# Optimization experiments

Measured on AMD Instinct MI355X. Metric: run time of the kernel, lower is better.

## Reference

```python
import jax, jax.numpy as jnp
import numpy as np

NUM_CLASSES = 8
EPS = 1e-4  # variance epsilon from the original module
MARGIN = 1.0  # __init__ arg; unused in the forward math


def setup_inputs() -> dict:
    key = jax.random.key(0)
    kf, kl = jax.random.split(key)
    features = jax.random.normal(kf, (65536, 2, 256), dtype=jnp.float32)
    labels = jax.random.randint(kl, (65536,), 0, NUM_CLASSES)
    return {"features": features, "labels": labels}


def _loss(features, labels):
    B, V, D = features.shape
    # Views of each sample are stacked into the sample's class group
    X = features.reshape(B * V, D)              # [N, D]
    lab = jnp.repeat(labels, V)                 # [N]
    onehot = (lab[:, None] == jnp.arange(NUM_CLASSES)[None, :]).astype(X.dtype)  # [N, C]

    counts = onehot.sum(axis=0)                 # [C] per-class row counts (all > 1 by construction)
    sums = onehot.T @ X                         # [C, D]
    means = sums / counts[:, None]              # [C, D]
    e2 = onehot.T @ (X * X)                     # [C, D] per-class sum of squares
    # unbiased per-feature variance (torch.var default, ddof=1)
    var = (e2 - counts[:, None] * means * means) / (counts[:, None] - 1.0)
    std = jnp.sqrt(var + EPS)
    std_loss = jnp.sum(jnp.mean(jax.nn.relu(1.0 - std), axis=1))  # sum over classes of mean over features

    # Per-class covariance: cov_c = (X_c - mu_c)^T (X_c - mu_c) / (n_c - 1)
    #                             = (sum_c x x^T - n_c mu mu^T) / (n_c - 1)
    S = jnp.einsum('nc,nd,ne->cde', onehot, X, X)  # [C, D, D]
    cov = (S - counts[:, None, None] * means[:, :, None] * means[:, None, :]) / (
        counts[:, None, None] - 1.0)
    diag = jnp.diagonal(cov, axis1=1, axis2=2)      # [C, D]
    offdiag_sq = jnp.sum(cov * cov, axis=(1, 2)) - jnp.sum(diag * diag, axis=1)
    cov_loss = jnp.sum(offdiag_sq / D)

    return std_loss + cov_loss


def reference(features, labels):
    return _loss(features, labels)
```

## Files before the change

kernel.cpp:

```cpp
#include <hip/hip_runtime.h>
#include <stdint.h>


#define NCLS  8
#define D     256
#define CHUNK 1024
#define SEG   256
#define EPSF  1e-4f
#define TMAX  144

typedef __bf16 bf16x8 __attribute__((ext_vector_type(8)));
typedef float  f32x4  __attribute__((ext_vector_type(4)));

__device__ __forceinline__ unsigned short f2bf(float f) {
    unsigned int x = __float_as_uint(f);
    x += 0x7fffu + ((x >> 16) & 1u);
    return (unsigned short)(x >> 16);
}

__global__ void k_hist(const int* __restrict__ labels, int nlab, int vfac,
                       int* __restrict__ counts) {
    __shared__ int lc[NCLS];
    int t = threadIdx.x;
    if (t < NCLS) lc[t] = 0;
    __syncthreads();
    for (int i = blockIdx.x * blockDim.x + t; i < nlab; i += gridDim.x * blockDim.x)
        atomicAdd(&lc[labels[i] & 7], vfac);
    __syncthreads();
    if (t < NCLS && lc[t]) atomicAdd(&counts[t], lc[t]);
}

__global__ void k_offsets(const int* __restrict__ counts,
                          int* __restrict__ offsets, int* __restrict__ cursor) {
    if (threadIdx.x == 0) {
        int acc = 0;
        for (int c = 0; c < NCLS; ++c) { offsets[c] = acc; cursor[c] = acc; acc += counts[c]; }
    }
}

__global__ __launch_bounds__(256) void k_idx(
    const int* __restrict__ labels, int nrows, int vfac,
    int* __restrict__ cursor, int* __restrict__ idx)
{
    __shared__ int lcnt[NCLS], lbase[NCLS];
    int t = threadIdx.x;
    int row = blockIdx.x * SEG + t;
    if (t < NCLS) lcnt[t] = 0;
    __syncthreads();
    int c = 0, rk = 0;
    bool ok = (row < nrows);
    if (ok) {
        c = labels[row / vfac] & 7;
        rk = atomicAdd(&lcnt[c], 1);
    }
    __syncthreads();
    if (t < NCLS) lbase[t] = lcnt[t] ? atomicAdd(&cursor[t], lcnt[t]) : 0;
    __syncthreads();
    if (ok) idx[lbase[c] + rk] = row;
}

__global__ __launch_bounds__(512) void k_gram_g(
    const float* __restrict__ X, const int* __restrict__ idx,
    const int* __restrict__ counts, const int* __restrict__ offsets,
    float* __restrict__ part, float* __restrict__ csums)
{
    __shared__ __align__(16) unsigned char lds[64 * 256 * 2];

    int t = threadIdx.x;
    int lane = t & 63;
    int w = t >> 6;
    int wrow = w >> 1;
    int wcol = w & 1;
    int kblk = t & 15;
    int cblk = t >> 4;

    int nch[NCLS], ofch[NCLS];
    int T = 0;
    for (int c = 0; c < NCLS; ++c) {
        int n = counts[c];
        nch[c] = (n + CHUNK - 1) / CHUNK;
        ofch[c] = T;
        T += nch[c];
    }

    const f32x4 zf = {0.f, 0.f, 0.f, 0.f};

    for (int wk = blockIdx.x; wk < 2 * T; wk += gridDim.x) {
        int item = wk >> 1;
        int half = wk & 1;
        int c = 0;
        while (c < NCLS - 1 && item >= ofch[c + 1]) ++c;
        int chunk = item - ofch[c];
        int base = offsets[c] + chunk * CHUNK;
        int rows = min(CHUNK, counts[c] - chunk * CHUNK);
        int ntiles = (rows + 63) >> 6;

        f32x4 acc[4][4];
        #pragma unroll
        for (int i = 0; i < 4; ++i)
            #pragma unroll
            for (int j = 0; j < 4; ++j)
                #pragma unroll
                for (int r = 0; r < 4; ++r) acc[i][j][r] = 0.f;
        float sumv[8];
        #pragma unroll
        for (int q = 0; q < 8; ++q) sumv[q] = 0.f;

        uint4 R[4];
        f32x4 fa[4], fb[4];
        int idn[4];

        #pragma unroll
        for (int j = 0; j < 4; ++j) {
            int r = kblk * 4 + j;
            idn[j] = (r < rows) ? idx[base + r] : 0;
        }
        #pragma unroll
        for (int j = 0; j < 4; ++j) {
            int r = kblk * 4 + j;
            if (r < rows) {
                const float* rp = X + ((size_t)idn[j] << 8) + cblk * 8;
                fa[j] = *(const f32x4*)rp;
                fb[j] = *(const f32x4*)(rp + 4);
            } else { fa[j] = zf; fb[j] = zf; }
        }
        #pragma unroll
        for (int j = 0; j < 4; ++j) {
            int r = 64 + kblk * 4 + j;
            idn[j] = (r < rows) ? idx[base + r] : 0;
        }
        #pragma unroll
        for (int j = 0; j < 4; ++j) {
            #pragma unroll
            for (int q = 0; q < 4; ++q) { sumv[q] += fa[j][q]; sumv[4 + q] += fb[j][q]; }
            unsigned int w0 = (unsigned int)f2bf(fa[j][0]) | ((unsigned int)f2bf(fa[j][1]) << 16);
            unsigned int w1 = (unsigned int)f2bf(fa[j][2]) | ((unsigned int)f2bf(fa[j][3]) << 16);
            unsigned int w2 = (unsigned int)f2bf(fb[j][0]) | ((unsigned int)f2bf(fb[j][1]) << 16);
            unsigned int w3 = (unsigned int)f2bf(fb[j][2]) | ((unsigned int)f2bf(fb[j][3]) << 16);
            R[j] = make_uint4(w0, w1, w2, w3);
        }

        for (int kt = 0; kt < ntiles; ++kt) {
            __syncthreads();
            #pragma unroll
            for (int cc = 0; cc < 8; ++cc) {
                int wd = cc >> 1;
                int sh = (cc & 1) * 16;
                unsigned int e0 = (((const unsigned int*)&R[0])[wd] >> sh) & 0xffffu;
                unsigned int e1 = (((const unsigned int*)&R[1])[wd] >> sh) & 0xffffu;
                unsigned int e2 = (((const unsigned int*)&R[2])[wd] >> sh) & 0xffffu;
                unsigned int e3 = (((const unsigned int*)&R[3])[wd] >> sh) & 0xffffu;
                int ccol = cblk * 8 + cc;
                int byt = ccol * 128 + ((kblk * 8) ^ (cc << 4));
                *(uint2*)(lds + byt) = make_uint2(e0 | (e1 << 16), e2 | (e3 << 16));
            }
            __syncthreads();

            bool more = (kt + 1 < ntiles);
            if (more) {
                #pragma unroll
                for (int j = 0; j < 4; ++j) {
                    int r = (kt + 1) * 64 + kblk * 4 + j;
                    if (r < rows) {
                        const float* rp = X + ((size_t)idn[j] << 8) + cblk * 8;
                        fa[j] = *(const f32x4*)rp;
                        fb[j] = *(const f32x4*)(rp + 4);
                    } else { fa[j] = zf; fb[j] = zf; }
                }
            }
            int idf[4];
            #pragma unroll
            for (int j = 0; j < 4; ++j) {
                int r = (kt + 2) * 64 + kblk * 4 + j;
                idf[j] = (more && r < rows) ? idx[base + r] : 0;
            }
            __builtin_amdgcn_sched_barrier(0);

            #pragma unroll
            for (int ks = 0; ks < 2; ++ks) {
                int kb2 = ks * 64 + ((lane >> 4) << 4);
                int swz = (lane & 7) << 4;
                bf16x8 bfr[4];
                #pragma unroll
                for (int tj = 0; tj < 4; ++tj) {
                    int ccol = half * 128 + wcol * 64 + tj * 16 + (lane & 15);
                    bfr[tj] = __builtin_bit_cast(bf16x8,
                        *(const uint4*)(lds + ccol * 128 + (kb2 ^ swz)));
                }
                #pragma unroll
                for (int ti = 0; ti < 4; ++ti) {
                    int ccol = wrow * 64 + ti * 16 + (lane & 15);
                    bf16x8 af = __builtin_bit_cast(bf16x8,
                        *(const uint4*)(lds + ccol * 128 + (kb2 ^ swz)));
                    #pragma unroll
                    for (int tj = 0; tj < 4; ++tj)
                        acc[ti][tj] = __builtin_amdgcn_mfma_f32_16x16x32_bf16(
                            af, bfr[tj], acc[ti][tj], 0, 0, 0);
                }
            }

            if (more) {
                #pragma unroll
                for (int j = 0; j < 4; ++j) {
                    #pragma unroll
                    for (int q = 0; q < 4; ++q) { sumv[q] += fa[j][q]; sumv[4 + q] += fb[j][q]; }
                    unsigned int w0 = (unsigned int)f2bf(fa[j][0]) | ((unsigned int)f2bf(fa[j][1]) << 16);
                    unsigned int w1 = (unsigned int)f2bf(fa[j][2]) | ((unsigned int)f2bf(fa[j][3]) << 16);
                    unsigned int w2 = (unsigned int)f2bf(fb[j][0]) | ((unsigned int)f2bf(fb[j][1]) << 16);
                    unsigned int w3 = (unsigned int)f2bf(fb[j][2]) | ((unsigned int)f2bf(fb[j][3]) << 16);
                    R[j] = make_uint4(w0, w1, w2, w3);
                }
                #pragma unroll
                for (int j = 0; j < 4; ++j) idn[j] = idf[j];
            }
        }

        float* dst = part + (size_t)item * (D * D);
        #pragma unroll
        for (int ti = 0; ti < 4; ++ti) {
            int row0 = wrow * 64 + ti * 16 + ((lane >> 4) << 2);
            #pragma unroll
            for (int tj = 0; tj < 4; ++tj) {
                int col = half * 128 + wcol * 64 + tj * 16 + (lane & 15);
                #pragma unroll
                for (int r = 0; r < 4; ++r)
                    dst[(row0 + r) * D + col] = acc[ti][tj][r];
            }
        }

        #pragma unroll
        for (int s = 1; s < 16; s <<= 1)
            #pragma unroll
            for (int q = 0; q < 8; ++q)
                sumv[q] += __shfl_xor(sumv[q], s, 64);
        if (half == 0 && (t & 15) == 0) {
            float* cs = csums + (size_t)item * D + cblk * 8;
            #pragma unroll
            for (int q = 0; q < 8; ++q) cs[q] = sumv[q];
        }
        __syncthreads();
    }
}

__global__ __launch_bounds__(256) void k_gsum(
    const float* __restrict__ csums, const int* __restrict__ counts,
    float* __restrict__ gsums)
{
    int c = blockIdx.x;
    int i = threadIdx.x;
    int of = 0;
    for (int cc = 0; cc < c; ++cc) of += (counts[cc] + CHUNK - 1) / CHUNK;
    int nc = (counts[c] + CHUNK - 1) / CHUNK;
    float s = 0.f;
    for (int q = 0; q < nc; ++q) s += csums[(size_t)(of + q) * D + i];
    gsums[c * D + i] = s;
}

__global__ __launch_bounds__(256) void k_loss(
    const float* __restrict__ part, const float* __restrict__ gsums,
    const int* __restrict__ counts, float* __restrict__ out)
{
    __shared__ float red[256];
    int t = threadIdx.x;
    int nch[NCLS], ofch[NCLS];
    int T = 0;
    for (int c = 0; c < NCLS; ++c) {
        int n = counts[c];
        nch[c] = (n + CHUNK - 1) / CHUNK;
        ofch[c] = T;
        T += nch[c];
    }
    float local = 0.f;
    const int total = NCLS * D * D;
    for (int idx = blockIdx.x * blockDim.x + t; idx < total; idx += gridDim.x * blockDim.x) {
        int c = idx >> 16;
        int ij = idx & 0xffff;
        int i = ij >> 8, j = ij & 255;
        const float* p = part + (size_t)ofch[c] * (D * D) + ij;
        float s = 0.f;
        for (int q = 0; q < nch[c]; ++q) s += p[(size_t)q * (D * D)];
        float n  = (float)counts[c];
        float mi = gsums[c * D + i] / n;
        float mj = gsums[c * D + j] / n;
        float cov = (s - n * mi * mj) / (n - 1.f);
        float contrib;
        if (i == j) {
            float sd = sqrtf(cov + EPSF);
            contrib = fmaxf(1.f - sd, 0.f) * (1.f / (float)D);
        } else {
            contrib = cov * cov * (1.f / (float)D);
        }
        local += contrib;
    }
    red[t] = local;
    __syncthreads();
    for (int s = 128; s > 0; s >>= 1) {
        if (t < s) red[t] += red[t + s];
        __syncthreads();
    }
    if (t == 0) atomicAdd(out, red[0]);
}

extern "C" void kernel_launch(void* const* d_in, const int* in_sizes, int n_in,
                              void* d_out, int out_size, void* d_ws, size_t ws_size,
                              hipStream_t stream)
{
    const float* X      = (const float*)d_in[0];
    const int*   labels = (const int*)d_in[1];
    int nfeat = in_sizes[0];
    int nlab  = in_sizes[1];
    int nrows = nfeat / D;
    int vfac  = nrows / nlab;

    char* ws = (char*)d_ws;
    size_t off_idx   = 0;
    size_t sz_idx    = (size_t)nrows * 4;
    size_t off_part  = (off_idx + sz_idx + 255) & ~(size_t)255;
    size_t sz_part   = (size_t)TMAX * D * D * 4;
    size_t off_cs    = (off_part + sz_part + 255) & ~(size_t)255;
    size_t sz_cs     = (size_t)TMAX * D * 4;
    size_t off_gs    = (off_cs + sz_cs + 255) & ~(size_t)255;
    size_t sz_gs     = (size_t)NCLS * D * 4;
    size_t off_cnt   = (off_gs + sz_gs + 255) & ~(size_t)255;
    size_t off_ofs   = off_cnt + 64;
    size_t off_cur   = off_ofs + 64;

    int*   idx     = (int*)(ws + off_idx);
    float* part    = (float*)(ws + off_part);
    float* csums   = (float*)(ws + off_cs);
    float* gsums   = (float*)(ws + off_gs);
    int*   counts  = (int*)(ws + off_cnt);
    int*   offsets = (int*)(ws + off_ofs);
    int*   cursor  = (int*)(ws + off_cur);

    hipMemsetAsync(counts, 0, 64, stream);
    hipMemsetAsync(d_out, 0, (size_t)out_size * sizeof(float), stream);

    k_hist<<<64, 256, 0, stream>>>(labels, nlab, vfac, counts);
    k_offsets<<<1, 64, 0, stream>>>(counts, offsets, cursor);
    k_idx<<<(nrows + SEG - 1) / SEG, SEG, 0, stream>>>(labels, nrows, vfac, cursor, idx);
    k_gram_g<<<2 * TMAX, 512, 0, stream>>>(X, idx, counts, offsets, part, csums);
    k_gsum<<<NCLS, 256, 0, stream>>>(csums, counts, gsums);
    k_loss<<<512, 256, 0, stream>>>(part, gsums, counts, (float*)d_out);
}
```

Measured before the change: 125.8 us.

## Double-buffer LDS tiles in gram kernel to drop one barrier per k-step

The shared-memory staging buffer for the bf16 row tiles becomes double-buffered. Each iteration computes MFMAs from the current buffer while the next tile is converted and written into the other buffer, so only one __syncthreads per k-step is needed instead of two. Row-bounds branches on gathers are replaced by clamped indices plus masking after the load, which makes the loads unconditional. The cost is double the LDS footprint (64KB per block), which may reduce occupancy, plus extra redundant loads for tail rows.

```diff
diff --git a/kernel.cpp b/kernel.cpp
--- a/kernel.cpp
+++ b/kernel.cpp
@@ -64,7 +64,7 @@
     const int* __restrict__ counts, const int* __restrict__ offsets,
     float* __restrict__ part, float* __restrict__ csums)
 {
-    __shared__ __align__(16) unsigned char lds[64 * 256 * 2];
+    __shared__ __align__(16) unsigned char lds[2][64 * 256 * 2];
 
     int t = threadIdx.x;
     int lane = t & 63;
@@ -106,28 +106,23 @@
         #pragma unroll
         for (int q = 0; q < 8; ++q) sumv[q] = 0.f;
 
+        f32x4 fa[4], fb[4];
         uint4 R[4];
-        f32x4 fa[4], fb[4];
         int idn[4];
 
         #pragma unroll
         for (int j = 0; j < 4; ++j) {
             int r = kblk * 4 + j;
-            idn[j] = (r < rows) ? idx[base + r] : 0;
-        }
-        #pragma unroll
-        for (int j = 0; j < 4; ++j) {
-            int r = kblk * 4 + j;
-            if (r < rows) {
-                const float* rp = X + ((size_t)idn[j] << 8) + cblk * 8;
-                fa[j] = *(const f32x4*)rp;
-                fb[j] = *(const f32x4*)(rp + 4);
-            } else { fa[j] = zf; fb[j] = zf; }
+            int rid = idx[base + min(r, rows - 1)];
+            const float* rp = X + ((size_t)rid << 8) + cblk * 8;
+            fa[j] = *(const f32x4*)rp;
+            fb[j] = *(const f32x4*)(rp + 4);
+            if (r >= rows) { fa[j] = zf; fb[j] = zf; }
         }
         #pragma unroll
         for (int j = 0; j < 4; ++j) {
             int r = 64 + kblk * 4 + j;
-            idn[j] = (r < rows) ? idx[base + r] : 0;
+            idn[j] = idx[base + min(r, rows - 1)];
         }
         #pragma unroll
         for (int j = 0; j < 4; ++j) {
@@ -139,43 +134,98 @@
             unsigned int w3 = (unsigned int)f2bf(fb[j][2]) | ((unsigned int)f2bf(fb[j][3]) << 16);
             R[j] = make_uint4(w0, w1, w2, w3);
         }
-
-        for (int kt = 0; kt < ntiles; ++kt) {
-            __syncthreads();
-            #pragma unroll
-            for (int cc = 0; cc < 8; ++cc) {
-                int wd = cc >> 1;
-                int sh = (cc & 1) * 16;
-                unsigned int e0 = (((const unsigned int*)&R[0])[wd] >> sh) & 0xffffu;
-                unsigned int e1 = (((const unsigned int*)&R[1])[wd] >> sh) & 0xffffu;
-                unsigned int e2 = (((const unsigned int*)&R[2])[wd] >> sh) & 0xffffu;
-                unsigned int e3 = (((const unsigned int*)&R[3])[wd] >> sh) & 0xffffu;
-                int ccol = cblk * 8 + cc;
-                int byt = ccol * 128 + ((kblk * 8) ^ (cc << 4));
-                *(uint2*)(lds + byt) = make_uint2(e0 | (e1 << 16), e2 | (e3 << 16));
-            }
-            __syncthreads();
-
-            bool more = (kt + 1 < ntiles);
-            if (more) {
-                #pragma unroll
-                for (int j = 0; j < 4; ++j) {
-                    int r = (kt + 1) * 64 + kblk * 4 + j;
-                    if (r < rows) {
-                        const float* rp = X + ((size_t)idn[j] << 8) + cblk * 8;
-                        fa[j] = *(const f32x4*)rp;
-                        fb[j] = *(const f32x4*)(rp + 4);
-                    } else { fa[j] = zf; fb[j] = zf; }
-                }
-            }
-            int idf[4];
+        #pragma unroll
+        for (int cc = 0; cc < 8; ++cc) {
+            int wd = cc >> 1;
+            int sh = (cc & 1) * 16;
+            unsigned int e0 = (((const unsigned int*)&R[0])[wd] >> sh) & 0xffffu;
+            unsigned int e1 = (((const unsigned int*)&R[1])[wd] >> sh) & 0xffffu;
+            unsigned int e2 = (((const unsigned int*)&R[2])[wd] >> sh) & 0xffffu;
+            unsigned int e3 = (((const unsigned int*)&R[3])[wd] >> sh) & 0xffffu;
+            int ccol = cblk * 8 + cc;
+            int byt = ccol * 128 + ((kblk * 8) ^ (cc << 4));
+            *(uint2*)(&lds[0][0] + byt) = make_uint2(e0 | (e1 << 16), e2 | (e3 << 16));
+        }
+        __syncthreads();
+
+        int ntm1 = ntiles - 1;
+        for (int kt = 0; kt < ntm1; ++kt) {
+            int cur = kt & 1;
+            #pragma unroll
+            for (int j = 0; j < 4; ++j) {
+                const float* rp = X + ((size_t)idn[j] << 8) + cblk * 8;
+                fa[j] = *(const f32x4*)rp;
+                fb[j] = *(const f32x4*)(rp + 4);
+            }
+            int idnn[4];
             #pragma unroll
             for (int j = 0; j < 4; ++j) {
                 int r = (kt + 2) * 64 + kblk * 4 + j;
-                idf[j] = (more && r < rows) ? idx[base + r] : 0;
+                idnn[j] = idx[base + min(r, rows - 1)];
             }
             __builtin_amdgcn_sched_barrier(0);
 
+            {
+                const unsigned char* lb = &lds[0][0] + cur * 32768;
+                #pragma unroll
+                for (int ks = 0; ks < 2; ++ks) {
+                    int kb2 = ks * 64 + ((lane >> 4) << 4);
+                    int swz = (lane & 7) << 4;
+                    bf16x8 bfr[4];
+                    #pragma unroll
+                    for (int tj = 0; tj < 4; ++tj) {
+                        int ccol = half * 128 + wcol * 64 + tj * 16 + (lane & 15);
+                        bfr[tj] = __builtin_bit_cast(bf16x8,
+                            *(const uint4*)(lb + ccol * 128 + (kb2 ^ swz)));
+                    }
+                    #pragma unroll
+                    for (int ti = 0; ti < 4; ++ti) {
+                        int ccol = wrow * 64 + ti * 16 + (lane & 15);
+                        bf16x8 af = __builtin_bit_cast(bf16x8,
+                            *(const uint4*)(lb + ccol * 128 + (kb2 ^ swz)));
+                        #pragma unroll
+                        for (int tj = 0; tj < 4; ++tj)
+                            acc[ti][tj] = __builtin_amdgcn_mfma_f32_16x16x32_bf16(
+                                af, bfr[tj], acc[ti][tj], 0, 0, 0);
+                    }
+                }
+            }
+            __builtin_amdgcn_sched_barrier(0);
+
+            #pragma unroll
+            for (int j = 0; j < 4; ++j) {
+                int r = (kt + 1) * 64 + kblk * 4 + j;
+                if (r >= rows) { fa[j] = zf; fb[j] = zf; }
+                #pragma unroll
+                for (int q = 0; q < 4; ++q) { sumv[q] += fa[j][q]; sumv[4 + q] += fb[j][q]; }
+                unsigned int w0 = (unsigned int)f2bf(fa[j][0]) | ((unsigned int)f2bf(fa[j][1]) << 16);
+                unsigned int w1 = (unsigned int)f2bf(fa[j][2]) | ((unsigned int)f2bf(fa[j][3]) << 16);
+                unsigned int w2 = (unsigned int)f2bf(fb[j][0]) | ((unsigned int)f2bf(fb[j][1]) << 16);
+                unsigned int w3 = (unsigned int)f2bf(fb[j][2]) | ((unsigned int)f2bf(fb[j][3]) << 16);
+                R[j] = make_uint4(w0, w1, w2, w3);
+            }
+            {
+                unsigned char* wb = &lds[0][0] + (cur ^ 1) * 32768;
+                #pragma unroll
+                for (int cc = 0; cc < 8; ++cc) {
+                    int wd = cc >> 1;
+                    int sh = (cc & 1) * 16;
+                    unsigned int e0 = (((const unsigned int*)&R[0])[wd] >> sh) & 0xffffu;
+                    unsigned int e1 = (((const unsigned int*)&R[1])[wd] >> sh) & 0xffffu;
+                    unsigned int e2 = (((const unsigned int*)&R[2])[wd] >> sh) & 0xffffu;
+                    unsigned int e3 = (((const unsigned int*)&R[3])[wd] >> sh) & 0xffffu;
+                    int ccol = cblk * 8 + cc;
+                    int byt = ccol * 128 + ((kblk * 8) ^ (cc << 4));
+                    *(uint2*)(wb + byt) = make_uint2(e0 | (e1 << 16), e2 | (e3 << 16));
+                }
+            }
+            #pragma unroll
+            for (int j = 0; j < 4; ++j) idn[j] = idnn[j];
+            __syncthreads();
+        }
+
+        {
+            const unsigned char* lb = &lds[0][0] + (ntm1 & 1) * 32768;
             #pragma unroll
             for (int ks = 0; ks < 2; ++ks) {
                 int kb2 = ks * 64 + ((lane >> 4) << 4);
@@ -185,33 +235,18 @@
                 for (int tj = 0; tj < 4; ++tj) {
                     int ccol = half * 128 + wcol * 64 + tj * 16 + (lane & 15);
                     bfr[tj] = __builtin_bit_cast(bf16x8,
-                        *(const uint4*)(lds + ccol * 128 + (kb2 ^ swz)));
+                        *(const uint4*)(lb + ccol * 128 + (kb2 ^ swz)));
                 }
                 #pragma unroll
                 for (int ti = 0; ti < 4; ++ti) {
                     int ccol = wrow * 64 + ti * 16 + (lane & 15);
                     bf16x8 af = __builtin_bit_cast(bf16x8,
-                        *(const uint4*)(lds + ccol * 128 + (kb2 ^ swz)));
+                        *(const uint4*)(lb + ccol * 128 + (kb2 ^ swz)));
                     #pragma unroll
                     for (int tj = 0; tj < 4; ++tj)
                         acc[ti][tj] = __builtin_amdgcn_mfma_f32_16x16x32_bf16(
                             af, bfr[tj], acc[ti][tj], 0, 0, 0);
                 }
-            }
-
-            if (more) {
-                #pragma unroll
-                for (int j = 0; j < 4; ++j) {
-                    #pragma unroll
-                    for (int q = 0; q < 4; ++q) { sumv[q] += fa[j][q]; sumv[4 + q] += fb[j][q]; }
-                    unsigned int w0 = (unsigned int)f2bf(fa[j][0]) | ((unsigned int)f2bf(fa[j][1]) << 16);
-                    unsigned int w1 = (unsigned int)f2bf(fa[j][2]) | ((unsigned int)f2bf(fa[j][3]) << 16);
-                    unsigned int w2 = (unsigned int)f2bf(fb[j][0]) | ((unsigned int)f2bf(fb[j][1]) << 16);
-                    unsigned int w3 = (unsigned int)f2bf(fb[j][2]) | ((unsigned int)f2bf(fb[j][3]) << 16);
-                    R[j] = make_uint4(w0, w1, w2, w3);
-                }
-                #pragma unroll
-                for (int j = 0; j < 4; ++j) idn[j] = idf[j];
             }
         }
 
```

Measured after the change: 115.5 us. 8.1% less time.
